# Performance work log

Measured on AMD Instinct MI355X. Metric: run time of the kernel, lower is better.

## Reference

```python
import jax, jax.numpy as jnp
import numpy as np

B, Q, H = 1, 1024, 2048
NH, NKV, HD = 32, 8, 64
KB = 2048
THETA = 10000.0
KB_MAX_TRAIN = 4096.0


def _bitlinear(x, w):
    """BitNet b1.58 linear: per-token int8 absmax activation quant + ternary weight quant (STE)."""
    a_scale = 127.0 / jnp.clip(jnp.max(jnp.abs(x), axis=-1, keepdims=True), 1e-5)
    xq = jnp.clip(jnp.round(x * a_scale), -128.0, 127.0) / a_scale
    w_scale = 1.0 / jnp.clip(jnp.mean(jnp.abs(w)), 1e-5)
    wq = jnp.clip(jnp.round(w * w_scale), -1.0, 1.0) / w_scale
    x_ste = x + jax.lax.stop_gradient(xq - x)
    w_ste = w + jax.lax.stop_gradient(wq - w)
    return jnp.einsum('bsh,oh->bso', x_ste, w_ste)


def _rope_cos_sin(position_ids):
    inv_freq = 1.0 / (THETA ** (jnp.arange(0, HD, 2, dtype=jnp.float32) / HD))  # [HD/2]
    freqs = position_ids.astype(jnp.float32)[..., None] * inv_freq  # [B,Q,HD/2]
    emb = jnp.concatenate([freqs, freqs], axis=-1)  # [B,Q,HD]
    return jnp.cos(emb)[:, None], jnp.sin(emb)[:, None]  # [B,1,Q,HD]


def _rotate_half(x):
    return jnp.concatenate([-x[..., HD // 2:], x[..., :HD // 2]], axis=-1)


def setup_inputs() -> dict:
    key = jax.random.key(0)
    ks = jax.random.split(key, 9)
    hidden_states = jax.random.normal(ks[0], (B, Q, H), jnp.float32)
    # additive causal mask
    attention_mask = jnp.triu(jnp.full((Q, Q), -1e9, jnp.float32), 1)[None, None]
    kb_keys = jax.random.normal(ks[1], (B, NH, KB, HD), jnp.float32)
    kb_values = jax.random.normal(ks[2], (B, NH, KB, HD), jnp.float32)
    s = 0.02
    Wq = jax.random.normal(ks[3], (NH * HD, H), jnp.float32) * s
    Wk = jax.random.normal(ks[4], (NKV * HD, H), jnp.float32) * s
    Wv = jax.random.normal(ks[5], (NKV * HD, H), jnp.float32) * s
    Wo = jax.random.normal(ks[6], (H, NH * HD), jnp.float32) * s
    Wq_new = jax.random.normal(ks[7], (NH * HD, H), jnp.float32) * s
    position_ids = jnp.arange(Q, dtype=jnp.int32)[None, :]
    return dict(hidden_states=hidden_states, attention_mask=attention_mask,
                kb_keys=kb_keys, kb_values=kb_values,
                Wq=Wq, Wk=Wk, Wv=Wv, Wo=Wo, Wq_new=Wq_new,
                position_ids=position_ids)


def reference(hidden_states, attention_mask, kb_keys, kb_values,
              Wq, Wk, Wv, Wo, Wq_new, position_ids):
    b, q_len, _ = hidden_states.shape
    # BitLinear QKV projections
    q = _bitlinear(hidden_states, Wq).reshape(b, q_len, NH, HD).transpose(0, 2, 1, 3)
    k = _bitlinear(hidden_states, Wk).reshape(b, q_len, NKV, HD).transpose(0, 2, 1, 3)
    v = _bitlinear(hidden_states, Wv).reshape(b, q_len, NKV, HD).transpose(0, 2, 1, 3)
    # RoPE on prompt q/k (KB query is NOT rotated, matching the source)
    cos, sin = _rope_cos_sin(position_ids)
    q = q * cos + _rotate_half(q) * sin
    k = k * cos + _rotate_half(k) * sin
    # GQA: repeat kv heads
    groups = NH // NKV
    k = jnp.repeat(k, groups, axis=1)
    v = jnp.repeat(v, groups, axis=1)
    # KB query via separate BitLinear
    kb_q = _bitlinear(hidden_states, Wq_new).reshape(b, q_len, NH, HD).transpose(0, 2, 1, 3)
    scale = 1.0 / jnp.sqrt(jnp.float32(HD))
    kb_len = kb_keys.shape[2]
    scores_kb = jnp.einsum('bhqd,bhkd->bhqk', kb_q, kb_keys) * scale
    scores_kb = scores_kb + (jnp.log(jnp.float32(KB_MAX_TRAIN)) - jnp.log(jnp.float32(kb_len)))
    scores_p = jnp.einsum('bhqd,bhkd->bhqk', q, k) * scale + attention_mask
    attn = jax.nn.softmax(jnp.concatenate([scores_kb, scores_p], axis=-1).astype(jnp.float32), axis=-1)
    out = (jnp.einsum('bhqk,bhkd->bhqd', attn[..., :kb_len], kb_values)
           + jnp.einsum('bhqk,bhkd->bhqd', attn[..., kb_len:], v))
    out = out.transpose(0, 2, 1, 3).reshape(b, q_len, NH * HD)
    return _bitlinear(out, Wo)
```

## Files before the change

### kernel.cpp

```cpp
#include <hip/hip_runtime.h>
#include <hip/hip_bf16.h>
#include <stdint.h>
#include <math.h>

#define cH    2048
#define cQ    1024
#define cNH   32
#define cNKV  8
#define cKB   2048

#define INV_BIG   (1.0f/4194304.0f)
#define INV_SMALL (1.0f/1048576.0f)

#define WS_SUMS 0
#define WS_DQ1  256
#define WS_DQ2  4352
#define WS_XQ   8448
#define WS_WALL 4202752
#define WS_QB   25174272
#define WS_KB   33562880
#define WS_VB   35660032
#define WS_QN   37757184
#define WS_ROPET 46145792

using short8  = __attribute__((ext_vector_type(8))) short;
using floatx4 = __attribute__((ext_vector_type(4))) float;

__device__ __forceinline__ void bsplit(float x, unsigned short& hi, unsigned short& lo) {
  __hip_bfloat16 h = __float2bfloat16(x);
  float hf = __bfloat162float(h);
  __hip_bfloat16 l = __float2bfloat16(x - hf);
  hi = *(unsigned short*)&h;
  lo = *(unsigned short*)&l;
}

__device__ __forceinline__ unsigned short tern(float v, float ws) {
  float q = rintf(v * ws);
  q = fminf(fmaxf(q, -1.0f), 1.0f);
  return (unsigned short)(__float_as_uint(q) >> 16);
}

__global__ void k_ropetab(const int* __restrict__ pos, float2* __restrict__ tab) {
  int i = blockIdx.x * 256 + threadIdx.x;
  int t = i >> 5, d = i & 31;
  double p = (double)pos[t];
  double ang = p * pow(10000.0, -(double)d / 32.0);
  tab[i] = make_float2((float)cos(ang), (float)sin(ang));
}

__global__ void k_abssum5(const float* __restrict__ w0, const float* __restrict__ w1,
                          const float* __restrict__ w2, const float* __restrict__ w3,
                          const float* __restrict__ w4, double* __restrict__ out) {
  __shared__ double red[256];
  const int seg = blockIdx.y;
  const float* w = seg == 0 ? w0 : seg == 1 ? w1 : seg == 2 ? w2 : seg == 3 ? w3 : w4;
  const int n4 = ((seg == 1 || seg == 2) ? 512 * 2048 : 2048 * 2048) / 4;
  double s = 0.0;
  for (int i = blockIdx.x * 256 + threadIdx.x; i < n4; i += gridDim.x * 256) {
    float4 x = *(const float4*)(w + (size_t)i * 4);
    s += (double)fabsf(x.x) + (double)fabsf(x.y) + (double)fabsf(x.z) + (double)fabsf(x.w);
  }
  red[threadIdx.x] = s;
  __syncthreads();
  for (int o = 128; o > 0; o >>= 1) {
    if ((int)threadIdx.x < o) red[threadIdx.x] += red[threadIdx.x + o];
    __syncthreads();
  }
  if (threadIdx.x == 0) atomicAdd(out + seg, red[0]);
}

__global__ void k_wquant4(const float* __restrict__ Wq, const float* __restrict__ Wk,
                          const float* __restrict__ Wv, const float* __restrict__ Wqn,
                          unsigned short* __restrict__ wall, const double* __restrict__ sums) {
  size_t i = ((size_t)blockIdx.x * 256 + threadIdx.x) * 4;
  const float* src; size_t off; double s; float inv;
  if (i < 4194304)      { src = Wq;  off = 0;       s = sums[0]; inv = INV_BIG; }
  else if (i < 5242880) { src = Wk;  off = 4194304; s = sums[1]; inv = INV_SMALL; }
  else if (i < 6291456) { src = Wv;  off = 5242880; s = sums[2]; inv = INV_SMALL; }
  else                  { src = Wqn; off = 6291456; s = sums[4]; inv = INV_BIG; }
  float ws = 1.0f / fmaxf((float)s * inv, 1e-5f);
  float4 x = *(const float4*)(src + (i - off));
  ushort4 o;
  o.x = tern(x.x, ws); o.y = tern(x.y, ws); o.z = tern(x.z, ws); o.w = tern(x.w, ws);
  *(ushort4*)(wall + i) = o;
}

__global__ void k_wquant(const float* __restrict__ w, unsigned short* __restrict__ wq,
                         const double* __restrict__ sum, float inv_n) {
  size_t i = ((size_t)blockIdx.x * 256 + threadIdx.x) * 4;
  float ws = 1.0f / fmaxf((float)(*sum) * inv_n, 1e-5f);
  float4 x = *(const float4*)(w + i);
  ushort4 o;
  o.x = tern(x.x, ws); o.y = tern(x.y, ws); o.z = tern(x.z, ws); o.w = tern(x.w, ws);
  *(ushort4*)(wq + i) = o;
}

__global__ void k_aquant(const float* __restrict__ x, unsigned short* __restrict__ xq,
                         float* __restrict__ dq, int K) {
  int t = blockIdx.x;
  const float4* xr = (const float4*)(x + (size_t)t * K);
  const int K4 = K / 4;
  __shared__ float red[256];
  float m = 0.0f;
  for (int i = threadIdx.x; i < K4; i += 256) {
    float4 v = xr[i];
    m = fmaxf(m, fmaxf(fmaxf(fabsf(v.x), fabsf(v.y)), fmaxf(fabsf(v.z), fabsf(v.w))));
  }
  red[threadIdx.x] = m;
  __syncthreads();
  for (int o = 128; o > 0; o >>= 1) {
    if ((int)threadIdx.x < o) red[threadIdx.x] = fmaxf(red[threadIdx.x], red[threadIdx.x + o]);
    __syncthreads();
  }
  float amax = fmaxf(red[0], 1e-5f);
  float as = 127.0f / amax;
  ushort4* xo = (ushort4*)(xq + (size_t)t * K);
  for (int i = threadIdx.x; i < K4; i += 256) {
    float4 v = xr[i];
    ushort4 o;
    float q;
    q = fminf(fmaxf(rintf(v.x * as), -128.0f), 127.0f); o.x = (unsigned short)(__float_as_uint(q) >> 16);
    q = fminf(fmaxf(rintf(v.y * as), -128.0f), 127.0f); o.y = (unsigned short)(__float_as_uint(q) >> 16);
    q = fminf(fmaxf(rintf(v.z * as), -128.0f), 127.0f); o.z = (unsigned short)(__float_as_uint(q) >> 16);
    q = fminf(fmaxf(rintf(v.w * as), -128.0f), 127.0f); o.w = (unsigned short)(__float_as_uint(q) >> 16);
    xo[i] = o;
  }
  if (threadIdx.x == 0) dq[t] = amax / 127.0f;
}

__global__ __launch_bounds__(256) void k_gemm_mfma(
    const unsigned short* __restrict__ Aq, const unsigned short* __restrict__ Ball,
    const float* __restrict__ adq, const double* __restrict__ sums,
    const float2* __restrict__ ropetab,
    float* __restrict__ oQ, float* __restrict__ oK,
    float* __restrict__ oV, float* __restrict__ oQN, int mode) {
  __shared__ unsigned short As[128 * 72];
  __shared__ unsigned short Bs[128 * 72];
  const int t = threadIdx.x;
  const int lane = t & 63;
  const int row16 = lane & 15, q = lane >> 4;
  const int w = t >> 6;
  const int wm = (w >> 1) * 64, wn = (w & 1) * 64;
  const int bx = blockIdx.x;
  const int m0 = blockIdx.y * 128;
  const unsigned short* Bp = Ball + (size_t)bx * 128 * 2048;

  floatx4 acc[4][4];
#pragma unroll
  for (int g = 0; g < 4; ++g)
#pragma unroll
    for (int h = 0; h < 4; ++h) acc[g][h] = (floatx4){0.f, 0.f, 0.f, 0.f};

  for (int k0 = 0; k0 < 2048; k0 += 64) {
#pragma unroll
    for (int i = 0; i < 4; ++i) {
      int c = t + 256 * i;
      int row = c >> 3, g8 = c & 7;
      *(uint4*)&As[row * 72 + g8 * 8] =
          *(const uint4*)(Aq + (size_t)(m0 + row) * 2048 + k0 + g8 * 8);
      *(uint4*)&Bs[row * 72 + g8 * 8] =
          *(const uint4*)(Bp + (size_t)row * 2048 + k0 + g8 * 8);
    }
    __syncthreads();
#pragma unroll
    for (int kk = 0; kk < 2; ++kk) {
      short8 af[4], bf[4];
#pragma unroll
      for (int g = 0; g < 4; ++g)
        af[g] = *(const short8*)&As[(wm + g * 16 + row16) * 72 + kk * 32 + q * 8];
#pragma unroll
      for (int h = 0; h < 4; ++h)
        bf[h] = *(const short8*)&Bs[(wn + h * 16 + row16) * 72 + kk * 32 + q * 8];
#pragma unroll
      for (int g = 0; g < 4; ++g)
#pragma unroll
        for (int h = 0; h < 4; ++h)
          acc[g][h] = __builtin_amdgcn_mfma_f32_16x16x32_bf16(af[g], bf[h], acc[g][h], 0, 0, 0);
    }
    __syncthreads();
  }

  float* outp; int Nout, nb0; float wdq;
  if (mode == 1)      { outp = oQ;  Nout = 2048; nb0 = bx * 128;        wdq = fmaxf((float)sums[3] * INV_BIG,   1e-5f); }
  else if (bx < 16)   { outp = oQ;  Nout = 2048; nb0 = bx * 128;        wdq = fmaxf((float)sums[0] * INV_BIG,   1e-5f); }
  else if (bx < 20)   { outp = oK;  Nout = 512;  nb0 = (bx - 16) * 128; wdq = fmaxf((float)sums[1] * INV_SMALL, 1e-5f); }
  else if (bx < 24)   { outp = oV;  Nout = 512;  nb0 = (bx - 20) * 128; wdq = fmaxf((float)sums[2] * INV_SMALL, 1e-5f); }
  else                { outp = oQN; Nout = 2048; nb0 = (bx - 24) * 128; wdq = fmaxf((float)sums[4] * INV_BIG,   1e-5f); }

  if (mode == 0 && bx < 20) {
#pragma unroll
    for (int g = 0; g < 4; ++g)
#pragma unroll
      for (int r = 0; r < 4; ++r) {
        int m = m0 + wm + g * 16 + q * 4 + r;
        float s = adq[m] * wdq;
        float2 cs0 = ropetab[m * 32 + row16];
        float2 cs1 = ropetab[m * 32 + 16 + row16];
        float v0 = acc[g][0][r] * s, v1 = acc[g][1][r] * s;
        float v2 = acc[g][2][r] * s, v3 = acc[g][3][r] * s;
        float o0 = v0 * cs0.x - v2 * cs0.y;
        float o2 = v2 * cs0.x + v0 * cs0.y;
        float o1 = v1 * cs1.x - v3 * cs1.y;
        float o3 = v3 * cs1.x + v1 * cs1.y;
        size_t base = (size_t)m * Nout + nb0 + wn;
        if (bx < 16) {
          outp[base + row16]      = o0;
          outp[base + 16 + row16] = o1;
          outp[base + 32 + row16] = o2;
          outp[base + 48 + row16] = o3;
        } else {
          unsigned int* ko = (unsigned int*)outp;
          unsigned short hi, lo;
          bsplit(o0, hi, lo); ko[base + row16]      = (unsigned int)hi | ((unsigned int)lo << 16);
          bsplit(o1, hi, lo); ko[base + 16 + row16] = (unsigned int)hi | ((unsigned int)lo << 16);
          bsplit(o2, hi, lo); ko[base + 32 + row16] = (unsigned int)hi | ((unsigned int)lo << 16);
          bsplit(o3, hi, lo); ko[base + 48 + row16] = (unsigned int)hi | ((unsigned int)lo << 16);
        }
      }
  } else {
#pragma unroll
    for (int g = 0; g < 4; ++g)
#pragma unroll
      for (int r = 0; r < 4; ++r) {
        int m = m0 + wm + g * 16 + q * 4 + r;
        float s = adq[m] * wdq;
#pragma unroll
        for (int h = 0; h < 4; ++h)
          outp[(size_t)m * Nout + nb0 + wn + h * 16 + row16] = acc[g][h][r] * s;
      }
  }
}

__global__ __launch_bounds__(256) void k_prep(
    const float* __restrict__ kbv, const float* __restrict__ Vb,
    unsigned int* __restrict__ vtKB, unsigned int* __restrict__ vtP,
    float* __restrict__ kbk) {
  __shared__ float Lf[64 * 65];
  const int b = blockIdx.x;
  if (b >= 1152) {
    int i = (b - 1152) * 1024 + threadIdx.x * 4;
    float4 x = *(const float4*)(kbk + i);
    unsigned short hi, lo;
    uint4 o;
    bsplit(x.x, hi, lo); o.x = (unsigned int)hi | ((unsigned int)lo << 16);
    bsplit(x.y, hi, lo); o.y = (unsigned int)hi | ((unsigned int)lo << 16);
    bsplit(x.z, hi, lo); o.z = (unsigned int)hi | ((unsigned int)lo << 16);
    bsplit(x.w, hi, lo); o.w = (unsigned int)hi | ((unsigned int)lo << 16);
    *(uint4*)((unsigned int*)kbk + i) = o;
    return;
  }
  const float* src; unsigned int* dst; int srcStride, dstStride;
  if (b < 1024) {
    int h = b >> 5, kt = b & 31;
    src = kbv + ((size_t)h * cKB + kt * 64) * 64;
    srcStride = 64;
    dst = vtKB + (size_t)(h * 64) * 2048 + kt * 64;
    dstStride = 2048;
  } else {
    int bb = b - 1024;
    int hkv = bb >> 4, kt = bb & 15;
    src = Vb + (size_t)(kt * 64) * 512 + hkv * 64;
    srcStride = 512;
    dst = vtP + (size_t)(hkv * 64) * 1024 + kt * 64;
    dstStride = 1024;
  }
  const int t = threadIdx.x;
#pragma unroll
  for (int i = 0; i < 4; ++i) {
    int c = t + 256 * i;
    int row = c >> 4, c4 = (c & 15) * 4;
    float4 x = *(const float4*)(src + (size_t)row * srcStride + c4);
    Lf[row * 65 + c4 + 0] = x.x;
    Lf[row * 65 + c4 + 1] = x.y;
    Lf[row * 65 + c4 + 2] = x.z;
    Lf[row * 65 + c4 + 3] = x.w;
  }
  __syncthreads();
  const int lane = t & 63, w = t >> 6;
#pragma unroll
  for (int it = 0; it < 16; ++it) {
    int d = w + 4 * it;
    float x = Lf[lane * 65 + d];
    unsigned short hi, lo;
    bsplit(x, hi, lo);
    dst[(size_t)d * dstStride + lane] = (unsigned int)hi | ((unsigned int)lo << 16);
  }
}

__global__ __launch_bounds__(256, 3) void k_attn_mfma(
    const float* __restrict__ Qr, float* qnctx,
    const unsigned int* __restrict__ Kp,
    const unsigned int* __restrict__ kbkP,
    const unsigned int* __restrict__ vtKB,
    const unsigned int* __restrict__ vtP) {
  __shared__ unsigned short Khi[64 * 72], Klo[64 * 72];
  __shared__ unsigned short Vhi[64 * 72], Vlo[64 * 72];
  __shared__ unsigned int   Pbuf[4][16 * 68];

  const int t = threadIdx.x;
  const int lane = t & 63;
  const int col = lane & 15;
  const int quad = lane >> 4;
  const int w = t >> 6;
  const int h = blockIdx.x;
  const int q0 = blockIdx.y * 64;
  const int hkv = h >> 2;
  const float kbbias = 0.69314718055994531f;
  unsigned int* Pw = &Pbuf[w][0];

  short8 qh[2], ql[2];
  auto load_q = [&](const float* base) {
#pragma unroll
    for (int kk = 0; kk < 2; ++kk) {
      const float* p = base + (size_t)(q0 + w * 16 + col) * 2048 + h * 64 + kk * 32 + quad * 8;
      float4 a = *(const float4*)p;
      float4 b = *(const float4*)(p + 4);
      float xs[8] = {a.x, a.y, a.z, a.w, b.x, b.y, b.z, b.w};
#pragma unroll
      for (int j = 0; j < 8; ++j) {
        unsigned short hi, lo;
        bsplit(xs[j] * 0.125f, hi, lo);
        qh[kk][j] = (short)hi;
        ql[kk][j] = (short)lo;
      }
    }
  };
  load_q(qnctx);

  floatx4 acco[4];
  float m_[4], l_[4];
#pragma unroll
  for (int nt = 0; nt < 4; ++nt) acco[nt] = (floatx4){0.f, 0.f, 0.f, 0.f};
#pragma unroll
  for (int r = 0; r < 4; ++r) { m_[r] = -3.0e38f; l_[r] = 0.f; }

  const int ntiles = 32 + (q0 >> 6) + 1;
  for (int kt = 0; kt < ntiles; ++kt) {
    const bool isKB = kt < 32;
    const int k0 = isKB ? kt * 64 : (kt - 32) * 64;
    if (kt == 32) load_q(Qr);

    {
      const unsigned int* ksrc = isKB ? kbkP + ((size_t)h * cKB + k0) * 64
                                      : Kp + (size_t)k0 * 512 + hkv * 64;
      const int kstride = isKB ? 64 : 512;
      const unsigned int* vsrc = isKB ? vtKB + (size_t)(h * 64) * 2048 + k0
                                      : vtP + (size_t)(hkv * 64) * 1024 + k0;
      const int vstride = isKB ? 2048 : 1024;
#pragma unroll
      for (int i = 0; i < 4; ++i) {
        int c = t + 256 * i;
        int row = c >> 4, c4 = (c & 15) * 4;
        uint4 v = *(const uint4*)(ksrc + (size_t)row * kstride + c4);
        *(uint2*)&Khi[row * 72 + c4] =
            make_uint2((v.x & 0xffffu) | (v.y << 16), (v.z & 0xffffu) | (v.w << 16));
        *(uint2*)&Klo[row * 72 + c4] =
            make_uint2((v.x >> 16) | (v.y & 0xffff0000u), (v.z >> 16) | (v.w & 0xffff0000u));
        uint4 u = *(const uint4*)(vsrc + (size_t)row * vstride + c4);
        *(uint2*)&Vhi[row * 72 + c4] =
            make_uint2((u.x & 0xffffu) | (u.y << 16), (u.z & 0xffffu) | (u.w << 16));
        *(uint2*)&Vlo[row * 72 + c4] =
            make_uint2((u.x >> 16) | (u.y & 0xffff0000u), (u.z >> 16) | (u.w & 0xffff0000u));
      }
    }
    __syncthreads();

    floatx4 accs[4];
#pragma unroll
    for (int nt = 0; nt < 4; ++nt) accs[nt] = (floatx4){0.f, 0.f, 0.f, 0.f};
#pragma unroll
    for (int kk = 0; kk < 2; ++kk) {
#pragma unroll
      for (int nt = 0; nt < 4; ++nt) {
        const int ko = (nt * 16 + col) * 72 + kk * 32 + quad * 8;
        short8 khh = *(const short8*)&Khi[ko];
        short8 kll = *(const short8*)&Klo[ko];
        accs[nt] = __builtin_amdgcn_mfma_f32_16x16x32_bf16(qh[kk], khh, accs[nt], 0, 0, 0);
        accs[nt] = __builtin_amdgcn_mfma_f32_16x16x32_bf16(ql[kk], khh, accs[nt], 0, 0, 0);
        accs[nt] = __builtin_amdgcn_mfma_f32_16x16x32_bf16(qh[kk], kll, accs[nt], 0, 0, 0);
      }
    }

    float sv[4][4];
#pragma unroll
    for (int nt = 0; nt < 4; ++nt) {
      int kg = k0 + nt * 16 + col;
#pragma unroll
      for (int r = 0; r < 4; ++r) {
        int qg = q0 + w * 16 + quad * 4 + r;
        float b = isKB ? kbbias : ((kg <= qg) ? 0.0f : -1e9f);
        sv[nt][r] = accs[nt][r] + b;
      }
    }
#pragma unroll
    for (int r = 0; r < 4; ++r) {
      float rmax = fmaxf(fmaxf(sv[0][r], sv[1][r]), fmaxf(sv[2][r], sv[3][r]));
#pragma unroll
      for (int off = 8; off; off >>= 1) rmax = fmaxf(rmax, __shfl_xor(rmax, off));
      float mnew = fmaxf(m_[r], rmax);
      float alpha = __expf(m_[r] - mnew);
      float psum = 0.f;
#pragma unroll
      for (int nt = 0; nt < 4; ++nt) {
        float p = __expf(sv[nt][r] - mnew);
        sv[nt][r] = p;
        psum += p;
      }
#pragma unroll
      for (int off = 8; off; off >>= 1) psum += __shfl_xor(psum, off);
      l_[r] = l_[r] * alpha + psum;
      m_[r] = mnew;
#pragma unroll
      for (int nt = 0; nt < 4; ++nt) acco[nt][r] *= alpha;
    }

#pragma unroll
    for (int nt = 0; nt < 4; ++nt)
#pragma unroll
      for (int r = 0; r < 4; ++r) {
        unsigned short ph, pl;
        bsplit(sv[nt][r], ph, pl);
        Pw[(quad * 4 + r) * 68 + nt * 16 + col] = (unsigned int)ph | ((unsigned int)pl << 16);
      }

#pragma unroll
    for (int kk = 0; kk < 2; ++kk) {
      uint4 pa = *(const uint4*)&Pw[col * 68 + kk * 32 + quad * 8];
      uint4 pb = *(const uint4*)&Pw[col * 68 + kk * 32 + quad * 8 + 4];
      union { unsigned int u[4]; short8 s; } uh, ul;
      uh.u[0] = (pa.x & 0xffffu) | (pa.y << 16);
      uh.u[1] = (pa.z & 0xffffu) | (pa.w << 16);
      uh.u[2] = (pb.x & 0xffffu) | (pb.y << 16);
      uh.u[3] = (pb.z & 0xffffu) | (pb.w << 16);
      ul.u[0] = (pa.x >> 16) | (pa.y & 0xffff0000u);
      ul.u[1] = (pa.z >> 16) | (pa.w & 0xffff0000u);
      ul.u[2] = (pb.x >> 16) | (pb.y & 0xffff0000u);
      ul.u[3] = (pb.z >> 16) | (pb.w & 0xffff0000u);
      short8 ph8 = uh.s, pl8 = ul.s;
#pragma unroll
      for (int nt = 0; nt < 4; ++nt) {
        const int vo = (nt * 16 + col) * 72 + kk * 32 + quad * 8;
        short8 vhh = *(const short8*)&Vhi[vo];
        short8 vll = *(const short8*)&Vlo[vo];
        acco[nt] = __builtin_amdgcn_mfma_f32_16x16x32_bf16(ph8, vhh, acco[nt], 0, 0, 0);
        acco[nt] = __builtin_amdgcn_mfma_f32_16x16x32_bf16(pl8, vhh, acco[nt], 0, 0, 0);
        acco[nt] = __builtin_amdgcn_mfma_f32_16x16x32_bf16(ph8, vll, acco[nt], 0, 0, 0);
      }
    }
    __syncthreads();
  }

#pragma unroll
  for (int r = 0; r < 4; ++r) {
    float linv = 1.0f / l_[r];
#pragma unroll
    for (int nt = 0; nt < 4; ++nt)
      qnctx[(size_t)(q0 + w * 16 + quad * 4 + r) * 2048 + h * 64 + nt * 16 + col] =
          acco[nt][r] * linv;
  }
}

extern "C" void kernel_launch(void* const* d_in, const int* in_sizes, int n_in,
                              void* d_out, int out_size, void* d_ws, size_t ws_size,
                              hipStream_t stream) {
  (void)in_sizes; (void)n_in; (void)out_size; (void)ws_size;
  const float* hidden = (const float*)d_in[0];
  float* kbk = (float*)d_in[2];
  const float* kbv = (const float*)d_in[3];
  const float* Wq  = (const float*)d_in[4];
  const float* Wk  = (const float*)d_in[5];
  const float* Wv  = (const float*)d_in[6];
  const float* Wo  = (const float*)d_in[7];
  const float* Wqn = (const float*)d_in[8];
  const int*   pos = (const int*)d_in[9];

  char* ws = (char*)d_ws;
  double* sums = (double*)(ws + WS_SUMS);
  float* dq1 = (float*)(ws + WS_DQ1);
  float* dq2 = (float*)(ws + WS_DQ2);
  unsigned short* xq   = (unsigned short*)(ws + WS_XQ);
  unsigned short* wall = (unsigned short*)(ws + WS_WALL);
  unsigned int* vtKB = (unsigned int*)(ws + WS_WALL);
  unsigned int* vtP  = (unsigned int*)(ws + WS_WALL + 16777216);
  unsigned short* wqo  = (unsigned short*)(ws + WS_QB);
  float* Qb  = (float*)(ws + WS_QB);
  float* Kb  = (float*)(ws + WS_KB);
  float* Vb  = (float*)(ws + WS_VB);
  float* QNC = (float*)(ws + WS_QN);
  float2* ropetab = (float2*)(ws + WS_ROPET);

  hipMemsetAsync(sums, 0, 64, stream);

  k_ropetab<<<128, 256, 0, stream>>>(pos, ropetab);
  k_abssum5<<<dim3(128, 5), 256, 0, stream>>>(Wq, Wk, Wv, Wo, Wqn, sums);
  k_wquant4<<<10240, 256, 0, stream>>>(Wq, Wk, Wv, Wqn, wall, sums);
  k_aquant<<<cQ, 256, 0, stream>>>(hidden, xq, dq1, cH);

  k_gemm_mfma<<<dim3(40, 8), 256, 0, stream>>>(xq, wall, dq1, sums, ropetab,
                                               Qb, Kb, Vb, QNC, 0);

  k_prep<<<1152 + 4096, 256, 0, stream>>>(kbv, Vb, vtKB, vtP, kbk);

  k_attn_mfma<<<dim3(cNH, cQ / 64), 256, 0, stream>>>(
      Qb, QNC, (const unsigned int*)Kb, (const unsigned int*)kbk, vtKB, vtP);

  k_wquant<<<4096, 256, 0, stream>>>(Wo, wqo, sums + 3, INV_BIG);
  k_aquant<<<cQ, 256, 0, stream>>>(QNC, xq, dq2, cH);

  k_gemm_mfma<<<dim3(16, 8), 256, 0, stream>>>(xq, wqo, dq2, sums, ropetab,
                                               (float*)d_out, nullptr, nullptr, nullptr, 1);
}
```

Measured before the change: 413.4 us.

## Pre-swizzle split bf16 K/V tiles and stage them via direct global-to-LDS loads

The K and V producers (QKV GEMM epilogue, k_prep, and the in-place KB-key conversion) now write separate hi/lo bf16 planes in per-64x64-tile layouts with an XOR swizzle. The attention kernel copies these tiles straight into LDS with global_load_lds 16-byte transfers and no register unpacking, and reads fragments with swizzled addresses instead of padded rows. The P hi/lo split also switches to bit-mask truncation, so the hi part is truncated rather than rounded. This aims to cut attention load-path instructions and LDS bank conflicts, at the cost of scattered 2-byte stores in the GEMM epilogue and a subtly different split numerics.

```diff
diff --git a/kernel.cpp b/kernel.cpp
--- a/kernel.cpp
+++ b/kernel.cpp
@@ -38,6 +38,11 @@
   float q = rintf(v * ws);
   q = fminf(fmaxf(q, -1.0f), 1.0f);
   return (unsigned short)(__float_as_uint(q) >> 16);
+}
+
+__device__ __forceinline__ void gload16(const void* g, void* l) {
+  __builtin_amdgcn_global_load_lds((const __attribute__((address_space(1))) void*)g,
+                                   (__attribute__((address_space(3))) void*)l, 16, 0, 0);
 }
 
 __global__ void k_ropetab(const int* __restrict__ pos, float2* __restrict__ tab) {
@@ -132,7 +137,8 @@
     const unsigned short* __restrict__ Aq, const unsigned short* __restrict__ Ball,
     const float* __restrict__ adq, const double* __restrict__ sums,
     const float2* __restrict__ ropetab,
-    float* __restrict__ oQ, float* __restrict__ oK,
+    float* __restrict__ oQ, unsigned short* __restrict__ oKhi,
+    unsigned short* __restrict__ oKlo,
     float* __restrict__ oV, float* __restrict__ oQN, int mode) {
   __shared__ unsigned short As[128 * 72];
   __shared__ unsigned short Bs[128 * 72];
@@ -180,10 +186,10 @@
     __syncthreads();
   }
 
-  float* outp; int Nout, nb0; float wdq;
+  float* outp = nullptr; int Nout = 0, nb0; float wdq;
   if (mode == 1)      { outp = oQ;  Nout = 2048; nb0 = bx * 128;        wdq = fmaxf((float)sums[3] * INV_BIG,   1e-5f); }
   else if (bx < 16)   { outp = oQ;  Nout = 2048; nb0 = bx * 128;        wdq = fmaxf((float)sums[0] * INV_BIG,   1e-5f); }
-  else if (bx < 20)   { outp = oK;  Nout = 512;  nb0 = (bx - 16) * 128; wdq = fmaxf((float)sums[1] * INV_SMALL, 1e-5f); }
+  else if (bx < 20)   {             Nout = 512;  nb0 = (bx - 16) * 128; wdq = fmaxf((float)sums[1] * INV_SMALL, 1e-5f); }
   else if (bx < 24)   { outp = oV;  Nout = 512;  nb0 = (bx - 20) * 128; wdq = fmaxf((float)sums[2] * INV_SMALL, 1e-5f); }
   else                { outp = oQN; Nout = 2048; nb0 = (bx - 24) * 128; wdq = fmaxf((float)sums[4] * INV_BIG,   1e-5f); }
 
@@ -202,19 +208,22 @@
         float o2 = v2 * cs0.x + v0 * cs0.y;
         float o1 = v1 * cs1.x - v3 * cs1.y;
         float o3 = v3 * cs1.x + v1 * cs1.y;
-        size_t base = (size_t)m * Nout + nb0 + wn;
         if (bx < 16) {
+          size_t base = (size_t)m * Nout + nb0 + wn;
           outp[base + row16]      = o0;
           outp[base + 16 + row16] = o1;
           outp[base + 32 + row16] = o2;
           outp[base + 48 + row16] = o3;
         } else {
-          unsigned int* ko = (unsigned int*)outp;
-          unsigned short hi, lo;
-          bsplit(o0, hi, lo); ko[base + row16]      = (unsigned int)hi | ((unsigned int)lo << 16);
-          bsplit(o1, hi, lo); ko[base + 16 + row16] = (unsigned int)hi | ((unsigned int)lo << 16);
-          bsplit(o2, hi, lo); ko[base + 32 + row16] = (unsigned int)hi | ((unsigned int)lo << 16);
-          bsplit(o3, hi, lo); ko[base + 48 + row16] = (unsigned int)hi | ((unsigned int)lo << 16);
+          int hkv_ = (nb0 + wn) >> 6;
+          int kt_ = m >> 6, rr = m & 63, sb = rr & 7;
+          size_t tb = ((size_t)(hkv_ * 16 + kt_)) * 4096 + (size_t)rr * 64;
+          int s0 = row16 >> 3, j0 = row16 & 7;
+          unsigned short hi, lo; int ix;
+          bsplit(o0, hi, lo); ix = (((0 + s0) ^ sb) << 3) + j0; oKhi[tb + ix] = hi; oKlo[tb + ix] = lo;
+          bsplit(o1, hi, lo); ix = (((2 + s0) ^ sb) << 3) + j0; oKhi[tb + ix] = hi; oKlo[tb + ix] = lo;
+          bsplit(o2, hi, lo); ix = (((4 + s0) ^ sb) << 3) + j0; oKhi[tb + ix] = hi; oKlo[tb + ix] = lo;
+          bsplit(o3, hi, lo); ix = (((6 + s0) ^ sb) << 3) + j0; oKhi[tb + ix] = hi; oKlo[tb + ix] = lo;
         }
       }
   } else {
@@ -233,38 +242,47 @@
 
 __global__ __launch_bounds__(256) void k_prep(
     const float* __restrict__ kbv, const float* __restrict__ Vb,
-    unsigned int* __restrict__ vtKB, unsigned int* __restrict__ vtP,
+    unsigned short* __restrict__ vtKBhi, unsigned short* __restrict__ vtPhi,
     float* __restrict__ kbk) {
+  const int b = blockIdx.x;
+  const int t = threadIdx.x;
+  if (b >= 1152) {
+    float* tile = kbk + (size_t)(b - 1152) * 4096;
+    float v[2][8];
+#pragma unroll
+    for (int u = 0; u < 2; ++u) {
+      int task = t + 256 * u;
+      int r = task >> 3, s = task & 7;
+      *(float4*)&v[u][0] = *(const float4*)(tile + r * 64 + s * 8);
+      *(float4*)&v[u][4] = *(const float4*)(tile + r * 64 + s * 8 + 4);
+    }
+    __syncthreads();
+    unsigned short* up = (unsigned short*)tile;
+#pragma unroll
+    for (int u = 0; u < 2; ++u) {
+      int task = t + 256 * u;
+      int r = task >> 3, s = task & 7;
+      union { unsigned short u16[8]; uint4 q; } hi, lo;
+#pragma unroll
+      for (int j = 0; j < 8; ++j) bsplit(v[u][j], hi.u16[j], lo.u16[j]);
+      size_t off = (size_t)r * 64 + ((s ^ (r & 7)) << 3);
+      *(uint4*)(up + off)        = hi.q;
+      *(uint4*)(up + 4096 + off) = lo.q;
+    }
+    return;
+  }
   __shared__ float Lf[64 * 65];
-  const int b = blockIdx.x;
-  if (b >= 1152) {
-    int i = (b - 1152) * 1024 + threadIdx.x * 4;
-    float4 x = *(const float4*)(kbk + i);
-    unsigned short hi, lo;
-    uint4 o;
-    bsplit(x.x, hi, lo); o.x = (unsigned int)hi | ((unsigned int)lo << 16);
-    bsplit(x.y, hi, lo); o.y = (unsigned int)hi | ((unsigned int)lo << 16);
-    bsplit(x.z, hi, lo); o.z = (unsigned int)hi | ((unsigned int)lo << 16);
-    bsplit(x.w, hi, lo); o.w = (unsigned int)hi | ((unsigned int)lo << 16);
-    *(uint4*)((unsigned int*)kbk + i) = o;
-    return;
-  }
-  const float* src; unsigned int* dst; int srcStride, dstStride;
+  const float* src; unsigned short *dhi, *dlo; int srcStride;
   if (b < 1024) {
     int h = b >> 5, kt = b & 31;
-    src = kbv + ((size_t)h * cKB + kt * 64) * 64;
-    srcStride = 64;
-    dst = vtKB + (size_t)(h * 64) * 2048 + kt * 64;
-    dstStride = 2048;
+    src = kbv + ((size_t)h * cKB + kt * 64) * 64; srcStride = 64;
+    dhi = vtKBhi + (size_t)b * 4096; dlo = dhi + 4194304;
   } else {
     int bb = b - 1024;
     int hkv = bb >> 4, kt = bb & 15;
-    src = Vb + (size_t)(kt * 64) * 512 + hkv * 64;
-    srcStride = 512;
-    dst = vtP + (size_t)(hkv * 64) * 1024 + kt * 64;
-    dstStride = 1024;
-  }
-  const int t = threadIdx.x;
+    src = Vb + (size_t)(kt * 64) * 512 + hkv * 64; srcStride = 512;
+    dhi = vtPhi + (size_t)bb * 4096; dlo = dhi + 524288;
+  }
 #pragma unroll
   for (int i = 0; i < 4; ++i) {
     int c = t + 256 * i;
@@ -276,26 +294,28 @@
     Lf[row * 65 + c4 + 3] = x.w;
   }
   __syncthreads();
-  const int lane = t & 63, w = t >> 6;
-#pragma unroll
-  for (int it = 0; it < 16; ++it) {
-    int d = w + 4 * it;
-    float x = Lf[lane * 65 + d];
-    unsigned short hi, lo;
-    bsplit(x, hi, lo);
-    dst[(size_t)d * dstStride + lane] = (unsigned int)hi | ((unsigned int)lo << 16);
+#pragma unroll
+  for (int u = 0; u < 2; ++u) {
+    int task = t + 256 * u;
+    int d = task >> 3, s = task & 7;
+    union { unsigned short u16[8]; uint4 q; } hi, lo;
+#pragma unroll
+    for (int j = 0; j < 8; ++j) bsplit(Lf[(s * 8 + j) * 65 + d], hi.u16[j], lo.u16[j]);
+    size_t off = (size_t)d * 64 + ((s ^ (d & 7)) << 3);
+    *(uint4*)(dhi + off) = hi.q;
+    *(uint4*)(dlo + off) = lo.q;
   }
 }
 
 __global__ __launch_bounds__(256, 3) void k_attn_mfma(
     const float* __restrict__ Qr, float* qnctx,
-    const unsigned int* __restrict__ Kp,
-    const unsigned int* __restrict__ kbkP,
-    const unsigned int* __restrict__ vtKB,
-    const unsigned int* __restrict__ vtP) {
-  __shared__ unsigned short Khi[64 * 72], Klo[64 * 72];
-  __shared__ unsigned short Vhi[64 * 72], Vlo[64 * 72];
-  __shared__ unsigned int   Pbuf[4][16 * 68];
+    const unsigned short* __restrict__ KPhi,
+    const unsigned short* __restrict__ kbkS,
+    const unsigned short* __restrict__ vtKBhi,
+    const unsigned short* __restrict__ vtPhi) {
+  __shared__ __attribute__((aligned(16))) unsigned short Khi[4096], Klo[4096];
+  __shared__ __attribute__((aligned(16))) unsigned short Vhi[4096], Vlo[4096];
+  __shared__ __attribute__((aligned(16))) unsigned int Pbuf[4][16 * 68];
 
   const int t = threadIdx.x;
   const int lane = t & 63;
@@ -307,6 +327,10 @@
   const int hkv = h >> 2;
   const float kbbias = 0.69314718055994531f;
   unsigned int* Pw = &Pbuf[w][0];
+  const int cb = col * 64;
+  const int sw0 = ((quad    ) ^ (col & 7)) << 3;
+  const int sw1 = ((quad + 4) ^ (col & 7)) << 3;
+  const int so = w * 1024 + lane * 8;
 
   short8 qh[2], ql[2];
   auto load_q = [&](const float* base) {
@@ -341,27 +365,24 @@
     if (kt == 32) load_q(Qr);
 
     {
-      const unsigned int* ksrc = isKB ? kbkP + ((size_t)h * cKB + k0) * 64
-                                      : Kp + (size_t)k0 * 512 + hkv * 64;
-      const int kstride = isKB ? 64 : 512;
-      const unsigned int* vsrc = isKB ? vtKB + (size_t)(h * 64) * 2048 + k0
-                                      : vtP + (size_t)(hkv * 64) * 1024 + k0;
-      const int vstride = isKB ? 2048 : 1024;
-#pragma unroll
-      for (int i = 0; i < 4; ++i) {
-        int c = t + 256 * i;
-        int row = c >> 4, c4 = (c & 15) * 4;
-        uint4 v = *(const uint4*)(ksrc + (size_t)row * kstride + c4);
-        *(uint2*)&Khi[row * 72 + c4] =
-            make_uint2((v.x & 0xffffu) | (v.y << 16), (v.z & 0xffffu) | (v.w << 16));
-        *(uint2*)&Klo[row * 72 + c4] =
-            make_uint2((v.x >> 16) | (v.y & 0xffff0000u), (v.z >> 16) | (v.w & 0xffff0000u));
-        uint4 u = *(const uint4*)(vsrc + (size_t)row * vstride + c4);
-        *(uint2*)&Vhi[row * 72 + c4] =
-            make_uint2((u.x & 0xffffu) | (u.y << 16), (u.z & 0xffffu) | (u.w << 16));
-        *(uint2*)&Vlo[row * 72 + c4] =
-            make_uint2((u.x >> 16) | (u.y & 0xffff0000u), (u.z >> 16) | (u.w & 0xffff0000u));
-      }
+      const unsigned short *sKhi, *sKlo, *sVhi, *sVlo;
+      if (isKB) {
+        const size_t tk = (size_t)(h * 32 + kt);
+        sKhi = kbkS + tk * 8192;   sKlo = sKhi + 4096;
+        sVhi = vtKBhi + tk * 4096; sVlo = sVhi + 4194304;
+      } else {
+        const size_t tk = (size_t)(hkv * 16 + (kt - 32));
+        sKhi = KPhi + tk * 4096;   sKlo = sKhi + 524288;
+        sVhi = vtPhi + tk * 4096;  sVlo = sVhi + 524288;
+      }
+      gload16(sKhi + so,       &Khi[w * 1024]);
+      gload16(sKhi + so + 512, &Khi[w * 1024 + 512]);
+      gload16(sKlo + so,       &Klo[w * 1024]);
+      gload16(sKlo + so + 512, &Klo[w * 1024 + 512]);
+      gload16(sVhi + so,       &Vhi[w * 1024]);
+      gload16(sVhi + so + 512, &Vhi[w * 1024 + 512]);
+      gload16(sVlo + so,       &Vlo[w * 1024]);
+      gload16(sVlo + so + 512, &Vlo[w * 1024 + 512]);
     }
     __syncthreads();
 
@@ -370,9 +391,10 @@
     for (int nt = 0; nt < 4; ++nt) accs[nt] = (floatx4){0.f, 0.f, 0.f, 0.f};
 #pragma unroll
     for (int kk = 0; kk < 2; ++kk) {
+      const int swk = kk ? sw1 : sw0;
 #pragma unroll
       for (int nt = 0; nt < 4; ++nt) {
-        const int ko = (nt * 16 + col) * 72 + kk * 32 + quad * 8;
+        const int ko = nt * 1024 + cb + swk;
         short8 khh = *(const short8*)&Khi[ko];
         short8 kll = *(const short8*)&Klo[ko];
         accs[nt] = __builtin_amdgcn_mfma_f32_16x16x32_bf16(qh[kk], khh, accs[nt], 0, 0, 0);
@@ -418,9 +440,10 @@
     for (int nt = 0; nt < 4; ++nt)
 #pragma unroll
       for (int r = 0; r < 4; ++r) {
-        unsigned short ph, pl;
-        bsplit(sv[nt][r], ph, pl);
-        Pw[(quad * 4 + r) * 68 + nt * 16 + col] = (unsigned int)ph | ((unsigned int)pl << 16);
+        unsigned xb = __float_as_uint(sv[nt][r]);
+        float hf = __uint_as_float(xb & 0xffff0000u);
+        unsigned db = __float_as_uint(sv[nt][r] - hf);
+        Pw[(quad * 4 + r) * 68 + nt * 16 + col] = (xb >> 16) | (db & 0xffff0000u);
       }
 
 #pragma unroll
@@ -437,9 +460,10 @@
       ul.u[2] = (pb.x >> 16) | (pb.y & 0xffff0000u);
       ul.u[3] = (pb.z >> 16) | (pb.w & 0xffff0000u);
       short8 ph8 = uh.s, pl8 = ul.s;
+      const int swk = kk ? sw1 : sw0;
 #pragma unroll
       for (int nt = 0; nt < 4; ++nt) {
-        const int vo = (nt * 16 + col) * 72 + kk * 32 + quad * 8;
+        const int vo = nt * 1024 + cb + swk;
         short8 vhh = *(const short8*)&Vhi[vo];
         short8 vll = *(const short8*)&Vlo[vo];
         acco[nt] = __builtin_amdgcn_mfma_f32_16x16x32_bf16(ph8, vhh, acco[nt], 0, 0, 0);
@@ -480,11 +504,12 @@
   float* dq2 = (float*)(ws + WS_DQ2);
   unsigned short* xq   = (unsigned short*)(ws + WS_XQ);
   unsigned short* wall = (unsigned short*)(ws + WS_WALL);
-  unsigned int* vtKB = (unsigned int*)(ws + WS_WALL);
-  unsigned int* vtP  = (unsigned int*)(ws + WS_WALL + 16777216);
+  unsigned short* vtKBhi = (unsigned short*)(ws + WS_WALL);
+  unsigned short* vtPhi  = (unsigned short*)(ws + WS_WALL + 16777216);
   unsigned short* wqo  = (unsigned short*)(ws + WS_QB);
   float* Qb  = (float*)(ws + WS_QB);
-  float* Kb  = (float*)(ws + WS_KB);
+  unsigned short* KPhi = (unsigned short*)(ws + WS_KB);
+  unsigned short* KPlo = KPhi + 524288;
   float* Vb  = (float*)(ws + WS_VB);
   float* QNC = (float*)(ws + WS_QN);
   float2* ropetab = (float2*)(ws + WS_ROPET);
@@ -497,16 +522,17 @@
   k_aquant<<<cQ, 256, 0, stream>>>(hidden, xq, dq1, cH);
 
   k_gemm_mfma<<<dim3(40, 8), 256, 0, stream>>>(xq, wall, dq1, sums, ropetab,
-                                               Qb, Kb, Vb, QNC, 0);
-
-  k_prep<<<1152 + 4096, 256, 0, stream>>>(kbv, Vb, vtKB, vtP, kbk);
+                                               Qb, KPhi, KPlo, Vb, QNC, 0);
+
+  k_prep<<<1152 + 1024, 256, 0, stream>>>(kbv, Vb, vtKBhi, vtPhi, kbk);
 
   k_attn_mfma<<<dim3(cNH, cQ / 64), 256, 0, stream>>>(
-      Qb, QNC, (const unsigned int*)Kb, (const unsigned int*)kbk, vtKB, vtP);
+      Qb, QNC, KPhi, (const unsigned short*)kbk, vtKBhi, vtPhi);
 
   k_wquant<<<4096, 256, 0, stream>>>(Wo, wqo, sums + 3, INV_BIG);
   k_aquant<<<cQ, 256, 0, stream>>>(QNC, xq, dq2, cH);
 
   k_gemm_mfma<<<dim3(16, 8), 256, 0, stream>>>(xq, wqo, dq2, sums, ropetab,
-                                               (float*)d_out, nullptr, nullptr, nullptr, 1);
-}
+                                               (float*)d_out, nullptr, nullptr,
+                                               nullptr, nullptr, 1);
+}
```

Measured after the change: 396.7 us. 1.04x faster.
